# Kernel optimization log

Hardware: AMD Instinct MI355X
Metric: run time of the kernel (lower is better)

The kernel has to match this reference:

```python
import jax, jax.numpy as jnp
import numpy as np

EPS = 1e-5

def _bn(x, g, b):
    # BatchNorm1d in training mode: biased batch variance, eps=1e-5
    mu = jnp.mean(x, axis=0)
    var = jnp.var(x, axis=0)
    return g * (x - mu) * jax.lax.rsqrt(var + EPS) + b

def _prelu(x, a):
    return jnp.where(x >= 0, x, a * x)

def setup_inputs() -> dict:
    key = jax.random.key(0)
    ks = jax.random.split(key, 32)
    B, MF, E = 4096, 128, 64
    f32 = jnp.float32

    def lin_w(k, o, i):
        bound = 1.0 / np.sqrt(i)
        return jax.random.uniform(k, (o, i), f32, -bound, bound)

    def lin_b(k, o, i):
        bound = 1.0 / np.sqrt(i)
        return jax.random.uniform(k, (o,), f32, -bound, bound)

    def exp_w(k, e, o, i):
        bound = 1.0 / np.sqrt(i)
        return jax.random.uniform(k, (e, o, i), f32, -bound, bound)

    def exp_b(k, e, o, i):
        bound = 1.0 / np.sqrt(i)
        return jax.random.uniform(k, (e, o), f32, -bound, bound)

    quarter = jnp.full((1,), 0.25, f32)  # PReLU default init
    return {
        'm0': jax.random.normal(ks[0], (B, MF), f32),
        'x0': jax.random.normal(ks[1], (B, 64), f32),
        'mW1': lin_w(ks[2], 256, 128), 'mb1': lin_b(ks[3], 256, 128),
        'mg1': jnp.ones((256,), f32), 'mbe1': jnp.zeros((256,), f32), 'ma1': quarter,
        'mW2': lin_w(ks[4], 128, 256), 'mb2': lin_b(ks[5], 128, 256),
        'mg2': jnp.ones((128,), f32), 'mbe2': jnp.zeros((128,), f32), 'ma2': quarter,
        'mW3': lin_w(ks[6], 64, 128), 'mb3': lin_b(ks[7], 64, 128),
        'mg3': jnp.ones((64,), f32), 'mbe3': jnp.zeros((64,), f32), 'ma3': quarter,
        'Wenc0': exp_w(ks[8], E, 256, 64), 'benc0': exp_b(ks[9], E, 256, 64),
        'Wenc1': exp_w(ks[10], E, 256, 256), 'benc1': exp_b(ks[11], E, 256, 256),
        'Wdec0': exp_w(ks[12], E, 256, 256), 'bdec0': exp_b(ks[13], E, 256, 256),
        'Wdec1': exp_w(ks[14], E, 64, 256), 'bdec1': exp_b(ks[15], E, 64, 256),
        'bng': jnp.ones((256,), f32), 'bnb': jnp.zeros((256,), f32), 'a': quarter,
    }

def reference(m0, x0, mW1, mb1, mg1, mbe1, ma1, mW2, mb2, mg2, mbe2, ma2,
              mW3, mb3, mg3, mbe3, ma3, Wenc0, benc0, Wenc1, benc1,
              Wdec0, bdec0, Wdec1, bdec1, bng, bnb, a):
    # m_encoder (MNet): Linear+BN+PReLU x3 -> per-sample expert weights [B, 64]
    h = _prelu(_bn(m0 @ mW1.T + mb1, mg1, mbe1), ma1)
    h = _prelu(_bn(h @ mW2.T + mb2, mg2, mbe2), ma2)
    w = _prelu(_bn(h @ mW3.T + mb3, mg3, mbe3), ma3)  # [B, E]

    w_sum = jnp.sum(w)           # scalar sum over all B*E, as in torch code
    wn = w / w_sum               # [B, E]

    def experts(z, W, b):
        # all-experts dense combine: sum_e wn[b,e] * (z @ W_e^T + b_e)
        h = jnp.einsum('bi,eoi->beo', z, W) + b  # [B, E, O]
        return jnp.einsum('beo,be->bo', h, wn)

    # encoder: depth=2, BN+PReLU after each layer (shared bn(256) and PReLU)
    z = _prelu(_bn(experts(x0, Wenc0, benc0), bng, bnb), a)
    z = _prelu(_bn(experts(z, Wenc1, benc1), bng, bnb), a)
    # decoder: BN+PReLU on all but last layer
    y = _prelu(_bn(experts(z, Wdec0, bdec0), bng, bnb), a)
    y = experts(y, Wdec1, bdec1)  # [B, 64]
    return y
```

## Files before the change

kernel.cpp:

```cpp
#include <hip/hip_runtime.h>
#include <stdint.h>

#define BATCH 4096
#define NEXP 64

typedef __bf16 bf16x8 __attribute__((ext_vector_type(8)));
typedef float f32x4 __attribute__((ext_vector_type(4)));
typedef float f32x8 __attribute__((ext_vector_type(8)));
typedef unsigned int u32x4 __attribute__((ext_vector_type(4)));
typedef unsigned short u16x4 __attribute__((ext_vector_type(4)));
typedef unsigned short u16x8 __attribute__((ext_vector_type(8)));

__device__ __forceinline__ unsigned short f2bf(float f) {
  unsigned u = __builtin_bit_cast(unsigned, f);
  u += 0x7fffu + ((u >> 16) & 1u);
  return (unsigned short)(u >> 16);
}

__device__ __forceinline__ void async_copy16(const void* g, void* l) {
  __builtin_amdgcn_global_load_lds(
      (const __attribute__((address_space(1))) void*)(uintptr_t)g,
      (__attribute__((address_space(3))) void*)(uintptr_t)l, 16, 0, 0);
}

enum { AM_PLAIN = 0, AM_BN = 1 };

template <int BM_, int BN_, int WR, int WC, int AMODE>
__global__ __launch_bounds__(256, 4) void gemm_k(
    const float* __restrict__ Af32, const float* __restrict__ scv,
    const float* __restrict__ shv, const float* __restrict__ alphaPtr,
    const unsigned short* __restrict__ PB, int K, int nsubsTot,
    float* __restrict__ Cp, const float* __restrict__ biasv, int N,
    int ktilesTot) {
  constexpr int MS = BM_ / 16;
  constexpr int NS = BN_ / 16;
  constexpr int WTM = BM_ / WR, WTN = BN_ / WC;
  constexpr int TM = WTM / 16, TN = WTN / 16;
  constexpr int PCH = MS / 2;

  __shared__ __align__(16) unsigned short As[2 * MS * 512];
  __shared__ __align__(16) unsigned short Bs[2 * NS * 512];

  const int tid = threadIdx.x;
  const int lane = tid & 63;
  const int wid = tid >> 6;
  const int wrow = wid / WC, wcol = wid % WC;

  const int m0 = blockIdx.x * BM_;
  const int ntile = blockIdx.y;
  const int n0 = ntile * BN_;

  float alpha = 0.f;
  if constexpr (AMODE == AM_BN) alpha = alphaPtr[0];

  f32x4 acc[TM][TN] = {};

  for (int kt = 0; kt < ktilesTot; ++kt) {
    const int k0 = kt * 64;

    for (int f = wid; f < 2 * NS; f += 4) {
      const int fkt = f / NS, fns = f % NS;
      const long fragIdx = (long)(k0 / 32 + fkt) * nsubsTot + (ntile * NS + fns);
      async_copy16(PB + fragIdx * 512 + lane * 8, &Bs[f * 512 + lane * 8]);
    }

#pragma unroll
    for (int p = 0; p < PCH; ++p) {
      const int id = p * 256 + tid;
      const int fA = id >> 6;
      const int q = id & 63;
      const int ksh = fA / MS, msub = fA % MS;
      const int kq = q >> 4, mrow = q & 15;
      const int m = msub * 16 + mrow;
      const int kg = k0 + ksh * 32 + kq * 8;
      const long mg = m0 + m;
      f32x8 vf;
      if constexpr (AMODE == AM_PLAIN) {
        const f32x4* src = (const f32x4*)(Af32 + mg * K + kg);
        f32x4 a0 = src[0], a1 = src[1];
#pragma unroll
        for (int j = 0; j < 4; ++j) { vf[j] = a0[j]; vf[4 + j] = a1[j]; }
      } else {
        const f32x4* src = (const f32x4*)(Af32 + mg * K + kg);
        f32x4 a0 = src[0], a1 = src[1];
        f32x4 s0 = *(const f32x4*)(scv + kg), s1 = *(const f32x4*)(scv + kg + 4);
        f32x4 h0 = *(const f32x4*)(shv + kg), h1 = *(const f32x4*)(shv + kg + 4);
#pragma unroll
        for (int j = 0; j < 4; ++j) {
          float v = fmaf(a0[j], s0[j], h0[j]);
          vf[j] = v >= 0.f ? v : alpha * v;
          float v2 = fmaf(a1[j], s1[j], h1[j]);
          vf[4 + j] = v2 >= 0.f ? v2 : alpha * v2;
        }
      }
      bf16x8 ob = __builtin_convertvector(vf, bf16x8);
      *(u16x8*)&As[id * 8] = __builtin_bit_cast(u16x8, ob);
    }
    __syncthreads();

#pragma unroll
    for (int ks = 0; ks < 2; ++ks) {
      bf16x8 af[TM], bfr[TN];
#pragma unroll
      for (int i = 0; i < TM; ++i) {
        const int msub = wrow * TM + i;
        af[i] = __builtin_bit_cast(
            bf16x8, *(const u32x4*)&As[(ks * MS + msub) * 512 + lane * 8]);
      }
#pragma unroll
      for (int j = 0; j < TN; ++j) {
        const int nsub = wcol * TN + j;
        bfr[j] = __builtin_bit_cast(
            bf16x8, *(const u32x4*)&Bs[(ks * NS + nsub) * 512 + lane * 8]);
      }
#pragma unroll
      for (int i = 0; i < TM; ++i)
#pragma unroll
        for (int j = 0; j < TN; ++j)
          acc[i][j] = __builtin_amdgcn_mfma_f32_16x16x32_bf16(af[i], bfr[j],
                                                              acc[i][j], 0, 0, 0);
    }
    __syncthreads();
  }

  const int q = lane >> 4, nn = lane & 15;
#pragma unroll
  for (int i = 0; i < TM; ++i) {
    const int rowb = m0 + wrow * WTM + i * 16 + q * 4;
#pragma unroll
    for (int j = 0; j < TN; ++j) {
      const int col = n0 + wcol * WTN + j * 16 + nn;
      const float bv = biasv ? biasv[col] : 0.f;
#pragma unroll
      for (int r = 0; r < 4; ++r)
        Cp[(long)(rowb + r) * N + col] = acc[i][j][r] + bv;
    }
  }
}

template <int BN_, int KE_, int EPB, int NTILE, int KHALVES>
__global__ __launch_bounds__(256, 2) void egemm_k(
    const unsigned short* __restrict__ zpk, const float* __restrict__ wnT,
    const float* __restrict__ bias, const unsigned short* __restrict__ PB,
    float* __restrict__ Cbase, long partStride, int N, int nsubsTot) {
  constexpr int KT2F = KE_ / 32;
  constexpr int KT2 = KT2F / KHALVES;
  constexpr int LK = (KT2 == 8) ? 3 : (KT2 == 4) ? 2 : 1;
  constexpr int NS = BN_ / 16;
  constexpr int TN = NS / 4;
  constexpr int TM = 4;
  constexpr int S = NEXP / EPB;
  constexpr int NC = NTILE * S * KHALVES;
  constexpr int T = EPB * KT2;
  constexpr int U = ((KT2 & 3) == 0) ? 1 : (4 / KT2);

  __shared__ __align__(16) unsigned short As[KT2 * 4 * 512];

  const int tid = threadIdx.x, lane = tid & 63, wid = tid >> 6;
  const int bx = blockIdx.x;
  const int combo = bx % NC;
  const int mb = bx / NC;
  const int ntile = combo % NTILE;
  const int rest = combo / NTILE;
  const int slice = rest % S;
  const int khalf = rest / S;
  const int e0 = slice * EPB;
  const int n0 = ntile * BN_;
  float* __restrict__ Cp = Cbase + (long)(khalf * S + slice) * partStride;
  const int nn = lane & 15, q = lane >> 4;
  const bool addBias = (KHALVES == 1) || (khalf == 0);

  {
    const unsigned short* zb =
        zpk + (long)mb * (KT2F * 4 * 512) + (long)khalf * (KT2 * 4 * 512);
    for (int f = wid; f < KT2 * 4; f += 4)
      async_copy16(zb + f * 512 + lane * 8, &As[f * 512 + lane * 8]);
  }

  const long kstr = (long)nsubsTot * 512;
  const unsigned short* Bq = PB + ((long)e0 * KT2F + khalf * KT2) * kstr +
                             ((long)ntile * NS + wid * TN) * 512 + lane * 8;
  auto baddr = [&](int u) {
    const int ei = u >> LK, kt = u & (KT2 - 1);
    return Bq + ((long)ei * KT2F + kt) * kstr;
  };

  u32x4 ring[4][TN];
#pragma unroll
  for (int t = 0; t < 4; ++t) {
    const unsigned short* a = baddr(t < T ? t : T - 1);
#pragma unroll
    for (int j = 0; j < TN; ++j) ring[t][j] = *(const u32x4*)(a + j * 512);
  }

  __syncthreads();

  f32x4 mainAcc[TM][TN] = {};

  for (int eb = 0; eb < EPB; eb += U) {
#pragma unroll
    for (int uu = 0; uu < U; ++uu) {
      const int ei = eb + uu;
      const int e = e0 + ei;
      f32x4 tmp[TM][TN];
#pragma unroll
      for (int j = 0; j < TN; ++j) {
        const float bv =
            addBias ? bias[(long)e * N + n0 + wid * (TN * 16) + j * 16 + nn]
                    : 0.f;
        f32x4 t4 = {bv, bv, bv, bv};
#pragma unroll
        for (int i = 0; i < TM; ++i) tmp[i][j] = t4;
      }
#pragma unroll
      for (int kt = 0; kt < KT2; ++kt) {
        const int slot = (uu * KT2 + kt) & 3;
#pragma unroll
        for (int i = 0; i < TM; ++i) {
          bf16x8 af = __builtin_bit_cast(
              bf16x8, *(const u32x4*)&As[(kt * 4 + i) * 512 + lane * 8]);
#pragma unroll
          for (int j = 0; j < TN; ++j)
            tmp[i][j] = __builtin_amdgcn_mfma_f32_16x16x32_bf16(
                af, __builtin_bit_cast(bf16x8, ring[slot][j]), tmp[i][j], 0, 0,
                0);
        }
        {
          const int u = ei * KT2 + kt;
          const int un = (u + 4 < T) ? (u + 4) : (T - 1);
          const unsigned short* a = baddr(un);
#pragma unroll
          for (int j = 0; j < TN; ++j)
            ring[slot][j] = *(const u32x4*)(a + j * 512);
        }
      }
#pragma unroll
      for (int i = 0; i < TM; ++i) {
        const int rowb = mb * 64 + i * 16 + q * 4;
        f32x4 wn4 = *(const f32x4*)(wnT + (long)e * BATCH + rowb);
#pragma unroll
        for (int j = 0; j < TN; ++j) mainAcc[i][j] += wn4 * tmp[i][j];
      }
    }
  }

#pragma unroll
  for (int i = 0; i < TM; ++i) {
    const int rowb = mb * 64 + i * 16 + q * 4;
#pragma unroll
    for (int j = 0; j < TN; ++j) {
      const int col = n0 + wid * (TN * 16) + j * 16 + nn;
#pragma unroll
      for (int r = 0; r < 4; ++r)
        Cp[(long)(rowb + r) * N + col] = mainAcc[i][j][r];
    }
  }
}

template <int NPARTS>
__global__ void hstats_k(float* __restrict__ P, long partStride,
                         f32x4* __restrict__ BS1, f32x4* __restrict__ BS2) {
  const int c0 = (threadIdx.x & 63) * 4;
  const int rg = threadIdx.x >> 6;
  const int rb = blockIdx.x * 8;
  f32x4 s = {0.f, 0.f, 0.f, 0.f}, s2 = {0.f, 0.f, 0.f, 0.f};
#pragma unroll
  for (int it = 0; it < 2; ++it) {
    const long r = rb + it * 4 + rg;
    f32x4 v[NPARTS];
#pragma unroll
    for (int p = 0; p < NPARTS; ++p)
      v[p] = *(const f32x4*)(P + p * partStride + r * 256 + c0);
    f32x4 x = v[0];
#pragma unroll
    for (int p = 1; p < NPARTS; ++p) x += v[p];
    *(f32x4*)(P + r * 256 + c0) = x;
    s += x;
    s2 += x * x;
  }
  __shared__ f32x4 sb[256], qb[256];
  sb[threadIdx.x] = s;
  qb[threadIdx.x] = s2;
  __syncthreads();
  if (threadIdx.x < 64) {
    f32x4 ts = sb[threadIdx.x] + sb[64 + threadIdx.x] + sb[128 + threadIdx.x] +
               sb[192 + threadIdx.x];
    f32x4 tq = qb[threadIdx.x] + qb[64 + threadIdx.x] + qb[128 + threadIdx.x] +
               qb[192 + threadIdx.x];
    BS1[threadIdx.x * 512 + blockIdx.x] = ts;
    BS2[threadIdx.x * 512 + blockIdx.x] = tq;
  }
}

__global__ void sfin_k(const f32x4* __restrict__ BS1,
                       const f32x4* __restrict__ BS2,
                       const float* __restrict__ g, const float* __restrict__ b,
                       float* __restrict__ scv, float* __restrict__ shv) {
  const int cg = blockIdx.x;
  f32x4 s1 = BS1[cg * 512 + threadIdx.x] + BS1[cg * 512 + 256 + threadIdx.x];
  f32x4 s2 = BS2[cg * 512 + threadIdx.x] + BS2[cg * 512 + 256 + threadIdx.x];
  __shared__ f32x4 sb[256], qb[256];
  sb[threadIdx.x] = s1;
  qb[threadIdx.x] = s2;
  __syncthreads();
  for (int st = 128; st > 0; st >>= 1) {
    if (threadIdx.x < st) {
      sb[threadIdx.x] += sb[threadIdx.x + st];
      qb[threadIdx.x] += qb[threadIdx.x + st];
    }
    __syncthreads();
  }
  if (threadIdx.x < 4) {
    const int c = cg * 4 + threadIdx.x;
    float mu = sb[0][threadIdx.x] * (1.f / BATCH);
    float var = qb[0][threadIdx.x] * (1.f / BATCH) - mu * mu;
    float isig = 1.f / sqrtf(var + 1e-5f);
    float sc_ = g[c] * isig;
    scv[c] = sc_;
    shv[c] = b[c] - mu * sc_;
  }
}

__global__ void stats_k(const float* __restrict__ H, int C,
                        const float* __restrict__ g, const float* __restrict__ b,
                        float* __restrict__ scv, float* __restrict__ shv) {
  const int c0 = blockIdx.x * 4;
  f32x4 s = {0.f, 0.f, 0.f, 0.f}, s2 = {0.f, 0.f, 0.f, 0.f};
  for (int r = threadIdx.x; r < BATCH; r += 256) {
    f32x4 x = *(const f32x4*)(H + (long)r * C + c0);
    s += x;
    s2 += x * x;
  }
  __shared__ f32x4 sb[256], qb[256];
  sb[threadIdx.x] = s;
  qb[threadIdx.x] = s2;
  __syncthreads();
  for (int st = 128; st > 0; st >>= 1) {
    if (threadIdx.x < st) {
      sb[threadIdx.x] += sb[threadIdx.x + st];
      qb[threadIdx.x] += qb[threadIdx.x + st];
    }
    __syncthreads();
  }
  if (threadIdx.x < 4) {
    const int c = c0 + threadIdx.x;
    float mu = sb[0][threadIdx.x] * (1.f / BATCH);
    float var = qb[0][threadIdx.x] * (1.f / BATCH) - mu * mu;
    float isig = 1.f / sqrtf(var + 1e-5f);
    float sc_ = g[c] * isig;
    scv[c] = sc_;
    shv[c] = b[c] - mu * sc_;
  }
}

__global__ void zbuild_pk(const float* __restrict__ H,
                          const float* __restrict__ scv,
                          const float* __restrict__ shv,
                          const float* __restrict__ alphaPtr,
                          unsigned short* __restrict__ zpk) {
  const int c = blockIdx.x * 256 + threadIdx.x;
  const float alpha = alphaPtr[0];
  const int mb = c >> 11, r = c & 2047;
  const int kt = r >> 8, q2 = r & 255;
  const int msub = q2 >> 6, ln = q2 & 63;
  const int row = mb * 64 + msub * 16 + (ln & 15);
  const int col = kt * 32 + (ln >> 4) * 8;
  const float* src = H + (long)row * 256 + col;
  f32x4 a0 = *(const f32x4*)src, a1 = *(const f32x4*)(src + 4);
  f32x4 s0 = *(const f32x4*)(scv + col), s1 = *(const f32x4*)(scv + col + 4);
  f32x4 h0 = *(const f32x4*)(shv + col), h1 = *(const f32x4*)(shv + col + 4);
  u16x8 o;
#pragma unroll
  for (int j = 0; j < 4; ++j) {
    float v = fmaf(a0[j], s0[j], h0[j]);
    v = v >= 0.f ? v : alpha * v;
    o[j] = f2bf(v);
    float v2 = fmaf(a1[j], s1[j], h1[j]);
    v2 = v2 >= 0.f ? v2 : alpha * v2;
    o[4 + j] = f2bf(v2);
  }
  *(u16x8*)(zpk + (long)c * 8) = o;
}

__global__ void wbuild_k(const float* __restrict__ G, const float* __restrict__ scv,
                         const float* __restrict__ shv,
                         const float* __restrict__ alphaPtr,
                         float* __restrict__ w, float* __restrict__ wps) {
  const int idx = blockIdx.x * 256 + threadIdx.x;
  const float alpha = alphaPtr[0];
  const int c0 = (idx * 4) & 63;
  f32x4 x = *(const f32x4*)(G + (long)idx * 4);
  f32x4 sv = *(const f32x4*)(scv + c0);
  f32x4 hv = *(const f32x4*)(shv + c0);
  f32x4 o;
  float part = 0.f;
#pragma unroll
  for (int j = 0; j < 4; ++j) {
    float v = fmaf(x[j], sv[j], hv[j]);
    v = v >= 0.f ? v : alpha * v;
    o[j] = v;
    part += v;
  }
  *(f32x4*)(w + (long)idx * 4) = o;
  __shared__ float sb[256];
  sb[threadIdx.x] = part;
  __syncthreads();
  for (int st = 128; st > 0; st >>= 1) {
    if (threadIdx.x < st) sb[threadIdx.x] += sb[threadIdx.x + st];
    __syncthreads();
  }
  if (threadIdx.x == 0) wps[blockIdx.x] = sb[0];
}

__global__ void wnTcast_k(const float* __restrict__ w,
                          const float* __restrict__ wps,
                          float* __restrict__ wnT, const float* __restrict__ x0,
                          unsigned short* __restrict__ x0pk) {
  const int bx = blockIdx.x;
  if (bx < 1024) {
    __shared__ float sb[256];
    sb[threadIdx.x] = wps[threadIdx.x];
    __syncthreads();
    for (int st = 128; st > 0; st >>= 1) {
      if (threadIdx.x < st) sb[threadIdx.x] += sb[threadIdx.x + st];
      __syncthreads();
    }
    const float inv = 1.0f / sb[0];
    const int idx = bx * 256 + threadIdx.x;
    const int e = idx >> 12, b2 = idx & 4095;
    wnT[idx] = w[(long)b2 * NEXP + e] * inv;
  } else {
    const int c = (bx - 1024) * 256 + threadIdx.x;
    const int mb = c >> 9, r = c & 511;
    const int kt = r >> 8, q2 = r & 255;
    const int msub = q2 >> 6, ln = q2 & 63;
    const int row = mb * 64 + msub * 16 + (ln & 15);
    const int col = kt * 32 + (ln >> 4) * 8;
    const float* src = x0 + (long)row * 64 + col;
    f32x4 a0 = *(const f32x4*)src, a1 = *(const f32x4*)(src + 4);
    u16x8 o;
#pragma unroll
    for (int j = 0; j < 4; ++j) {
      o[j] = f2bf(a0[j]);
      o[4 + j] = f2bf(a1[j]);
    }
    *(u16x8*)(x0pk + (long)c * 8) = o;
  }
}

__global__ void prepackall_k(
    const float* __restrict__ w0, const float* __restrict__ w1,
    const float* __restrict__ w2, const float* __restrict__ w3,
    const float* __restrict__ w4, const float* __restrict__ w5,
    const float* __restrict__ w6, unsigned short* __restrict__ PB) {
  const int t = blockIdx.x * 256 + threadIdx.x;
  const float* W;
  int nsubs, shI;
  long loc;
  if (t < 4096) { W = w0; nsubs = 16; shI = 7; loc = t; }
  else if (t < 8192) { W = w1; nsubs = 8; shI = 8; loc = t - 4096; }
  else if (t < 9216) { W = w2; nsubs = 4; shI = 7; loc = t - 8192; }
  else if (t < 140288) { W = w3; nsubs = 16; shI = 6; loc = t - 9216; }
  else if (t < 664576) { W = w4; nsubs = 16; shI = 8; loc = t - 140288; }
  else if (t < 1188864) { W = w5; nsubs = 16; shI = 8; loc = t - 664576; }
  else if (t < 1319936) { W = w6; nsubs = 4; shI = 8; loc = t - 1188864; }
  else return;
  const int lane = (int)(loc & 63);
  const long frag = loc >> 6;
  const int nsub = (int)(frag % nsubs);
  const long ktile = frag / nsubs;
  const int n = nsub * 16 + (lane & 15);
  const int k = (int)(ktile * 32 + (lane >> 4) * 8);
  const int e = k >> shI;
  const int i0 = k & ((1 << shI) - 1);
  const int O = nsubs * 16;
  const float* src = W + ((long)e * O + n) * (1 << shI) + i0;
  f32x4 a0 = *(const f32x4*)src, a1 = *(const f32x4*)(src + 4);
  u16x8 o;
#pragma unroll
  for (int j = 0; j < 4; ++j) {
    o[j] = f2bf(a0[j]);
    o[4 + j] = f2bf(a1[j]);
  }
  *(u16x8*)(PB + (long)t * 8) = o;
}

template <int NP>
__global__ void reduceN_k(const float* __restrict__ P, long partStride,
                          float* __restrict__ out, int total4) {
  const int idx = blockIdx.x * 256 + threadIdx.x;
  if (idx >= total4) return;
  f32x4 v[NP];
#pragma unroll
  for (int p = 0; p < NP; ++p)
    v[p] = *(const f32x4*)(P + p * partStride + (long)idx * 4);
  f32x4 s = v[0];
#pragma unroll
  for (int p = 1; p < NP; ++p) s += v[p];
  *(f32x4*)(out + (long)idx * 4) = s;
}

extern "C" void kernel_launch(void* const* d_in, const int* in_sizes, int n_in,
                              void* d_out, int out_size, void* d_ws, size_t ws_size,
                              hipStream_t stream) {
  const float* m0 = (const float*)d_in[0];
  const float* x0 = (const float*)d_in[1];
  const float* mW1 = (const float*)d_in[2];
  const float* mb1 = (const float*)d_in[3];
  const float* mg1 = (const float*)d_in[4];
  const float* mbe1 = (const float*)d_in[5];
  const float* ma1 = (const float*)d_in[6];
  const float* mW2 = (const float*)d_in[7];
  const float* mb2 = (const float*)d_in[8];
  const float* mg2 = (const float*)d_in[9];
  const float* mbe2 = (const float*)d_in[10];
  const float* ma2 = (const float*)d_in[11];
  const float* mW3 = (const float*)d_in[12];
  const float* mb3 = (const float*)d_in[13];
  const float* mg3 = (const float*)d_in[14];
  const float* mbe3 = (const float*)d_in[15];
  const float* ma3 = (const float*)d_in[16];
  const float* Wenc0 = (const float*)d_in[17];
  const float* benc0 = (const float*)d_in[18];
  const float* Wenc1 = (const float*)d_in[19];
  const float* benc1 = (const float*)d_in[20];
  const float* Wdec0 = (const float*)d_in[21];
  const float* bdec0 = (const float*)d_in[22];
  const float* Wdec1 = (const float*)d_in[23];
  const float* bdec1 = (const float*)d_in[24];
  const float* bng = (const float*)d_in[25];
  const float* bnb = (const float*)d_in[26];
  const float* aexp = (const float*)d_in[27];

  const long PSP = (long)BATCH * 256 + 64;
  const long PSD = (long)BATCH * 64 + 64;

  char* base = (char*)d_ws;
  size_t off = 0;
  auto alloc = [&](size_t bytes) {
    void* p = base + off;
    off = (off + bytes + 255) & ~(size_t)255;
    return p;
  };
  unsigned short* PB = (unsigned short*)alloc(1319936L * 16);
  const long CO_mW2 = 4096, CO_mW3 = 8192, CO_e0 = 9216, CO_e1 = 140288,
             CO_d0 = 664576, CO_d1 = 1188864;
  size_t pbElems = (size_t)(4 * PSP > 16 * PSD ? 4 * PSP : 16 * PSD);
  float* Pb = (float*)alloc(pbElems * 4);
  float* P0 = Pb;
  float* P1 = Pb + (long)BATCH * 256;
  unsigned short* zApk = (unsigned short*)alloc(BATCH * 256 * 2);
  unsigned short* zBpk = (unsigned short*)alloc(BATCH * 256 * 2);
  unsigned short* x0pk = (unsigned short*)alloc(BATCH * 64 * 2);
  float* wbuf = (float*)alloc(BATCH * 64 * 4);
  float* wnT = (float*)alloc((size_t)NEXP * BATCH * 4);
  f32x4* BS1 = (f32x4*)alloc(64 * 512 * 16);
  f32x4* BS2 = (f32x4*)alloc(64 * 512 * 16);
  float* scv = (float*)alloc(256 * 4);
  float* shv = (float*)alloc(256 * 4);
  float* wps = (float*)alloc(256 * 4);

  const dim3 blk(256);

  prepackall_k<<<5156, blk, 0, stream>>>(mW1, mW2, mW3, Wenc0, Wenc1, Wdec0,
                                         Wdec1, PB);

  gemm_k<64, 128, 2, 2, AM_PLAIN><<<dim3(64, 2, 1), blk, 0, stream>>>(
      m0, nullptr, nullptr, nullptr, PB, 128, 16, P0, mb1, 256, 2);
  stats_k<<<64, blk, 0, stream>>>(P0, 256, mg1, mbe1, scv, shv);
  gemm_k<64, 128, 2, 2, AM_BN><<<dim3(64, 1, 1), blk, 0, stream>>>(
      P0, scv, shv, ma1, PB + CO_mW2 * 8, 256, 8, P1, mb2, 128, 4);
  stats_k<<<32, blk, 0, stream>>>(P1, 128, mg2, mbe2, scv, shv);
  gemm_k<64, 64, 2, 2, AM_BN><<<dim3(64, 1, 1), blk, 0, stream>>>(
      P1, scv, shv, ma2, PB + CO_mW3 * 8, 128, 4, P0, mb3, 64, 2);
  stats_k<<<16, blk, 0, stream>>>(P0, 64, mg3, mbe3, scv, shv);
  wbuild_k<<<256, blk, 0, stream>>>(P0, scv, shv, ma3, wbuf, wps);
  wnTcast_k<<<1152, blk, 0, stream>>>(wbuf, wps, wnT, x0, x0pk);

  egemm_k<128, 64, 16, 2, 1><<<dim3(512), blk, 0, stream>>>(
      x0pk, wnT, benc0, PB + CO_e0 * 8, Pb, PSP, 256, 16);
  hstats_k<4><<<512, blk, 0, stream>>>(Pb, PSP, BS1, BS2);
  sfin_k<<<64, blk, 0, stream>>>(BS1, BS2, bng, bnb, scv, shv);
  zbuild_pk<<<512, blk, 0, stream>>>(Pb, scv, shv, aexp, zApk);

  egemm_k<128, 256, 32, 2, 2><<<dim3(512), blk, 0, stream>>>(
      zApk, wnT, benc1, PB + CO_e1 * 8, Pb, PSP, 256, 16);
  hstats_k<4><<<512, blk, 0, stream>>>(Pb, PSP, BS1, BS2);
  sfin_k<<<64, blk, 0, stream>>>(BS1, BS2, bng, bnb, scv, shv);
  zbuild_pk<<<512, blk, 0, stream>>>(Pb, scv, shv, aexp, zBpk);

  egemm_k<128, 256, 32, 2, 2><<<dim3(512), blk, 0, stream>>>(
      zBpk, wnT, bdec0, PB + CO_d0 * 8, Pb, PSP, 256, 16);
  hstats_k<4><<<512, blk, 0, stream>>>(Pb, PSP, BS1, BS2);
  sfin_k<<<64, blk, 0, stream>>>(BS1, BS2, bng, bnb, scv, shv);
  zbuild_pk<<<512, blk, 0, stream>>>(Pb, scv, shv, aexp, zApk);

  egemm_k<64, 256, 8, 1, 2><<<dim3(1024), blk, 0, stream>>>(
      zApk, wnT, bdec1, PB + CO_d1 * 8, Pb, PSD, 64, 4);
  reduceN_k<16><<<256, blk, 0, stream>>>(Pb, PSD, (float*)d_out, 65536);

  (void)in_sizes; (void)n_in; (void)out_size; (void)ws_size;
}
```

Before: 354.0 us.

## Switch expert GEMMs to fp16 MFMA, split weight prepack per layer, halve experts per block

Expert GEMM operands (activations and packed weights) now use fp16 instead of bf16 MFMA, and weight prepacking is split into per-layer launches that reuse one buffer instead of a single large prepack. Experts per block are halved with twice as many blocks, producing 8 partial sums instead of 4. Launch bounds rise to 4 waves per SIMD to raise occupancy, which tightens register limits. fp16 gives more mantissa precision but a narrower range, so large activations could overflow.

```diff
diff --git a/kernel.cpp b/kernel.cpp
--- a/kernel.cpp
+++ b/kernel.cpp
@@ -5,6 +5,7 @@
 #define NEXP 64
 
 typedef __bf16 bf16x8 __attribute__((ext_vector_type(8)));
+typedef _Float16 f16x8 __attribute__((ext_vector_type(8)));
 typedef float f32x4 __attribute__((ext_vector_type(4)));
 typedef float f32x8 __attribute__((ext_vector_type(8)));
 typedef unsigned int u32x4 __attribute__((ext_vector_type(4)));
@@ -15,6 +16,13 @@
   unsigned u = __builtin_bit_cast(unsigned, f);
   u += 0x7fffu + ((u >> 16) & 1u);
   return (unsigned short)(u >> 16);
+}
+__device__ __forceinline__ float bf2f(unsigned short h) {
+  unsigned u = ((unsigned)h) << 16;
+  return __builtin_bit_cast(float, u);
+}
+__device__ __forceinline__ unsigned short f2h(float f) {
+  return __builtin_bit_cast(unsigned short, (_Float16)f);
 }
 
 __device__ __forceinline__ void async_copy16(const void* g, void* l) {
@@ -139,7 +147,7 @@
 }
 
 template <int BN_, int KE_, int EPB, int NTILE, int KHALVES>
-__global__ __launch_bounds__(256, 2) void egemm_k(
+__global__ __launch_bounds__(256, 4) void egemm_k(
     const unsigned short* __restrict__ zpk, const float* __restrict__ wnT,
     const float* __restrict__ bias, const unsigned short* __restrict__ PB,
     float* __restrict__ Cbase, long partStride, int N, int nsubsTot) {
@@ -217,12 +225,12 @@
         const int slot = (uu * KT2 + kt) & 3;
 #pragma unroll
         for (int i = 0; i < TM; ++i) {
-          bf16x8 af = __builtin_bit_cast(
-              bf16x8, *(const u32x4*)&As[(kt * 4 + i) * 512 + lane * 8]);
+          f16x8 af = __builtin_bit_cast(
+              f16x8, *(const u32x4*)&As[(kt * 4 + i) * 512 + lane * 8]);
 #pragma unroll
           for (int j = 0; j < TN; ++j)
-            tmp[i][j] = __builtin_amdgcn_mfma_f32_16x16x32_bf16(
-                af, __builtin_bit_cast(bf16x8, ring[slot][j]), tmp[i][j], 0, 0,
+            tmp[i][j] = __builtin_amdgcn_mfma_f32_16x16x32_f16(
+                af, __builtin_bit_cast(f16x8, ring[slot][j]), tmp[i][j], 0, 0,
                 0);
         }
         {
@@ -374,10 +382,10 @@
   for (int j = 0; j < 4; ++j) {
     float v = fmaf(a0[j], s0[j], h0[j]);
     v = v >= 0.f ? v : alpha * v;
-    o[j] = f2bf(v);
+    o[j] = f2h(v);
     float v2 = fmaf(a1[j], s1[j], h1[j]);
     v2 = v2 >= 0.f ? v2 : alpha * v2;
-    o[4 + j] = f2bf(v2);
+    o[4 + j] = f2h(v2);
   }
   *(u16x8*)(zpk + (long)c * 8) = o;
 }
@@ -441,18 +449,17 @@
     u16x8 o;
 #pragma unroll
     for (int j = 0; j < 4; ++j) {
-      o[j] = f2bf(a0[j]);
-      o[4 + j] = f2bf(a1[j]);
+      o[j] = f2h(a0[j]);
+      o[4 + j] = f2h(a1[j]);
     }
     *(u16x8*)(x0pk + (long)c * 8) = o;
   }
 }
 
-__global__ void prepackall_k(
-    const float* __restrict__ w0, const float* __restrict__ w1,
-    const float* __restrict__ w2, const float* __restrict__ w3,
-    const float* __restrict__ w4, const float* __restrict__ w5,
-    const float* __restrict__ w6, unsigned short* __restrict__ PB) {
+__global__ void mnetprep_k(const float* __restrict__ w0,
+                           const float* __restrict__ w1,
+                           const float* __restrict__ w2,
+                           unsigned short* __restrict__ PB) {
   const int t = blockIdx.x * 256 + threadIdx.x;
   const float* W;
   int nsubs, shI;
@@ -460,10 +467,6 @@
   if (t < 4096) { W = w0; nsubs = 16; shI = 7; loc = t; }
   else if (t < 8192) { W = w1; nsubs = 8; shI = 8; loc = t - 4096; }
   else if (t < 9216) { W = w2; nsubs = 4; shI = 7; loc = t - 8192; }
-  else if (t < 140288) { W = w3; nsubs = 16; shI = 6; loc = t - 9216; }
-  else if (t < 664576) { W = w4; nsubs = 16; shI = 8; loc = t - 140288; }
-  else if (t < 1188864) { W = w5; nsubs = 16; shI = 8; loc = t - 664576; }
-  else if (t < 1319936) { W = w6; nsubs = 4; shI = 8; loc = t - 1188864; }
   else return;
   const int lane = (int)(loc & 63);
   const long frag = loc >> 6;
@@ -481,6 +484,31 @@
   for (int j = 0; j < 4; ++j) {
     o[j] = f2bf(a0[j]);
     o[4 + j] = f2bf(a1[j]);
+  }
+  *(u16x8*)(PB + (long)t * 8) = o;
+}
+
+__global__ void eprep_k(const float* __restrict__ W,
+                        unsigned short* __restrict__ PB, int nsubs, int shI,
+                        long totalChunks) {
+  const long t = (long)blockIdx.x * 256 + threadIdx.x;
+  if (t >= totalChunks) return;
+  const int lane = (int)(t & 63);
+  const long frag = t >> 6;
+  const int nsub = (int)(frag % nsubs);
+  const long ktile = frag / nsubs;
+  const int n = nsub * 16 + (lane & 15);
+  const int k = (int)(ktile * 32 + (lane >> 4) * 8);
+  const int e = k >> shI;
+  const int i0 = k & ((1 << shI) - 1);
+  const int O = nsubs * 16;
+  const float* src = W + ((long)e * O + n) * (1 << shI) + i0;
+  f32x4 a0 = *(const f32x4*)src, a1 = *(const f32x4*)(src + 4);
+  u16x8 o;
+#pragma unroll
+  for (int j = 0; j < 4; ++j) {
+    o[j] = f2h(a0[j]);
+    o[4 + j] = f2h(a1[j]);
   }
   *(u16x8*)(PB + (long)t * 8) = o;
 }
@@ -532,7 +560,7 @@
   const float* bnb = (const float*)d_in[26];
   const float* aexp = (const float*)d_in[27];
 
-  const long PSP = (long)BATCH * 256 + 64;
+  const long PSP32 = (long)BATCH * 256 + 64;
   const long PSD = (long)BATCH * 64 + 64;
 
   char* base = (char*)d_ws;
@@ -542,13 +570,14 @@
     off = (off + bytes + 255) & ~(size_t)255;
     return p;
   };
-  unsigned short* PB = (unsigned short*)alloc(1319936L * 16);
-  const long CO_mW2 = 4096, CO_mW3 = 8192, CO_e0 = 9216, CO_e1 = 140288,
-             CO_d0 = 664576, CO_d1 = 1188864;
-  size_t pbElems = (size_t)(4 * PSP > 16 * PSD ? 4 * PSP : 16 * PSD);
-  float* Pb = (float*)alloc(pbElems * 4);
-  float* P0 = Pb;
-  float* P1 = Pb + (long)BATCH * 256;
+  unsigned short* PBm = (unsigned short*)alloc(9216L * 16);
+  unsigned short* PBe = (unsigned short*)alloc(524288L * 16);
+  size_t pbBytes = 8UL * PSP32 * 4;
+  if (16UL * PSD * 4 > pbBytes) pbBytes = 16UL * PSD * 4;
+  void* PbBase = alloc(pbBytes);
+  float* Pb32 = (float*)PbBase;
+  float* P0 = Pb32;
+  float* P1 = Pb32 + (long)BATCH * 256;
   unsigned short* zApk = (unsigned short*)alloc(BATCH * 256 * 2);
   unsigned short* zBpk = (unsigned short*)alloc(BATCH * 256 * 2);
   unsigned short* x0pk = (unsigned short*)alloc(BATCH * 64 * 2);
@@ -562,42 +591,45 @@
 
   const dim3 blk(256);
 
-  prepackall_k<<<5156, blk, 0, stream>>>(mW1, mW2, mW3, Wenc0, Wenc1, Wdec0,
-                                         Wdec1, PB);
+  mnetprep_k<<<36, blk, 0, stream>>>(mW1, mW2, mW3, PBm);
 
   gemm_k<64, 128, 2, 2, AM_PLAIN><<<dim3(64, 2, 1), blk, 0, stream>>>(
-      m0, nullptr, nullptr, nullptr, PB, 128, 16, P0, mb1, 256, 2);
+      m0, nullptr, nullptr, nullptr, PBm, 128, 16, P0, mb1, 256, 2);
   stats_k<<<64, blk, 0, stream>>>(P0, 256, mg1, mbe1, scv, shv);
   gemm_k<64, 128, 2, 2, AM_BN><<<dim3(64, 1, 1), blk, 0, stream>>>(
-      P0, scv, shv, ma1, PB + CO_mW2 * 8, 256, 8, P1, mb2, 128, 4);
+      P0, scv, shv, ma1, PBm + 4096L * 8, 256, 8, P1, mb2, 128, 4);
   stats_k<<<32, blk, 0, stream>>>(P1, 128, mg2, mbe2, scv, shv);
   gemm_k<64, 64, 2, 2, AM_BN><<<dim3(64, 1, 1), blk, 0, stream>>>(
-      P1, scv, shv, ma2, PB + CO_mW3 * 8, 128, 4, P0, mb3, 64, 2);
+      P1, scv, shv, ma2, PBm + 8192L * 8, 128, 4, P0, mb3, 64, 2);
   stats_k<<<16, blk, 0, stream>>>(P0, 64, mg3, mbe3, scv, shv);
   wbuild_k<<<256, blk, 0, stream>>>(P0, scv, shv, ma3, wbuf, wps);
   wnTcast_k<<<1152, blk, 0, stream>>>(wbuf, wps, wnT, x0, x0pk);
 
-  egemm_k<128, 64, 16, 2, 1><<<dim3(512), blk, 0, stream>>>(
-      x0pk, wnT, benc0, PB + CO_e0 * 8, Pb, PSP, 256, 16);
-  hstats_k<4><<<512, blk, 0, stream>>>(Pb, PSP, BS1, BS2);
+  eprep_k<<<512, blk, 0, stream>>>(Wenc0, PBe, 16, 6, 131072);
+  egemm_k<128, 64, 8, 2, 1><<<dim3(1024), blk, 0, stream>>>(
+      x0pk, wnT, benc0, PBe, Pb32, PSP32, 256, 16);
+  hstats_k<8><<<512, blk, 0, stream>>>(Pb32, PSP32, BS1, BS2);
   sfin_k<<<64, blk, 0, stream>>>(BS1, BS2, bng, bnb, scv, shv);
-  zbuild_pk<<<512, blk, 0, stream>>>(Pb, scv, shv, aexp, zApk);
-
-  egemm_k<128, 256, 32, 2, 2><<<dim3(512), blk, 0, stream>>>(
-      zApk, wnT, benc1, PB + CO_e1 * 8, Pb, PSP, 256, 16);
-  hstats_k<4><<<512, blk, 0, stream>>>(Pb, PSP, BS1, BS2);
+  zbuild_pk<<<512, blk, 0, stream>>>(Pb32, scv, shv, aexp, zApk);
+
+  eprep_k<<<2048, blk, 0, stream>>>(Wenc1, PBe, 16, 8, 524288);
+  egemm_k<128, 256, 16, 2, 2><<<dim3(1024), blk, 0, stream>>>(
+      zApk, wnT, benc1, PBe, Pb32, PSP32, 256, 16);
+  hstats_k<8><<<512, blk, 0, stream>>>(Pb32, PSP32, BS1, BS2);
   sfin_k<<<64, blk, 0, stream>>>(BS1, BS2, bng, bnb, scv, shv);
-  zbuild_pk<<<512, blk, 0, stream>>>(Pb, scv, shv, aexp, zBpk);
-
-  egemm_k<128, 256, 32, 2, 2><<<dim3(512), blk, 0, stream>>>(
-      zBpk, wnT, bdec0, PB + CO_d0 * 8, Pb, PSP, 256, 16);
-  hstats_k<4><<<512, blk, 0, stream>>>(Pb, PSP, BS1, BS2);
+  zbuild_pk<<<512, blk, 0, stream>>>(Pb32, scv, shv, aexp, zBpk);
+
+  eprep_k<<<2048, blk, 0, stream>>>(Wdec0, PBe, 16, 8, 524288);
+  egemm_k<128, 256, 16, 2, 2><<<dim3(1024), blk, 0, stream>>>(
+      zBpk, wnT, bdec0, PBe, Pb32, PSP32, 256, 16);
+  hstats_k<8><<<512, blk, 0, stream>>>(Pb32, PSP32, BS1, BS2);
   sfin_k<<<64, blk, 0, stream>>>(BS1, BS2, bng, bnb, scv, shv);
-  zbuild_pk<<<512, blk, 0, stream>>>(Pb, scv, shv, aexp, zApk);
-
+  zbuild_pk<<<512, blk, 0, stream>>>(Pb32, scv, shv, aexp, zApk);
+
+  eprep_k<<<512, blk, 0, stream>>>(Wdec1, PBe, 4, 8, 131072);
   egemm_k<64, 256, 8, 1, 2><<<dim3(1024), blk, 0, stream>>>(
-      zApk, wnT, bdec1, PB + CO_d1 * 8, Pb, PSD, 64, 4);
-  reduceN_k<16><<<256, blk, 0, stream>>>(Pb, PSD, (float*)d_out, 65536);
+      zApk, wnT, bdec1, PBe, Pb32, PSD, 64, 4);
+  reduceN_k<16><<<256, blk, 0, stream>>>(Pb32, PSD, (float*)d_out, 65536);
 
   (void)in_sizes; (void)n_in; (void)out_size; (void)ws_size;
 }
```

New measurement: 613.9 us. 1.73x slower.
